# Kernel tuning notes

Measured on AMD Instinct MI355X. Metric: run time of the kernel, lower is better.

## Reference

```python
import jax, jax.numpy as jnp
import numpy as np

DIM = 128
DIM_OUT = 128
TK = 3   # time kernel (causal)
SK = 3   # spatial kernel
EPS = 1e-8


def setup_inputs() -> dict:
    key = jax.random.key(0)
    k1, k2, k3 = jax.random.split(key, 3)
    fmap = jax.random.normal(k1, (4, DIM, 16, 64, 64), dtype=jnp.float32)
    cond = jax.random.normal(k2, (4, DIM), dtype=jnp.float32)
    fan_in = DIM * TK * SK * SK
    gain = 0.75  # kaiming gain for selu
    weights = jax.random.normal(k3, (DIM_OUT, DIM, TK, SK, SK), dtype=jnp.float32) * (gain / np.sqrt(fan_in))
    return {"fmap": fmap, "cond": cond, "weights": weights}


def reference(fmap, cond, weights):
    # per-sample weight modulation: w[b,o,i,kt,kh,kw] = W[o,i,...] * (cond[b,i] + 1)
    w = weights[None] * (cond[:, None, :, None, None, None] + 1.0)
    # demodulation: normalize per (b, o) over (i, kt, kh, kw)
    ssq = jnp.sum(w * w, axis=(2, 3, 4, 5), keepdims=True)
    w = w * jax.lax.rsqrt(jnp.maximum(ssq, EPS))
    # causal time padding (TK-1, 0), symmetric spatial padding SK//2
    sp = SK // 2
    fmap_p = jnp.pad(fmap, ((0, 0), (0, 0), (TK - 1, 0), (sp, sp), (sp, sp)))
    # per-sample conv3d (equivalent to groups=b grouped conv)
    dn = ('NCDHW', 'OIDHW', 'NCDHW')
    def conv_one(x, wi):
        # x: [c, t, h, w], wi: [o, i, kt, kh, kw]
        return jax.lax.conv_general_dilated(
            x[None], wi, window_strides=(1, 1, 1), padding='VALID',
            dimension_numbers=dn)[0]
    return jax.vmap(conv_one)(fmap_p, w)  # [b, o, t, h, w]
```

## Files before the change

kernel.cpp:

```cpp
#include <hip/hip_runtime.h>

typedef float f32x4 __attribute__((ext_vector_type(4)));
typedef short s16x8 __attribute__((ext_vector_type(8)));

#define NB 4
#define CIN 128
#define COUT 128
#define NT 16
#define NH 64
#define NW 64
#define NTAP 27
#define KTOT (CIN * NTAP)

#define FT_H 66
#define FT_W 66
#define WMOD_BYTES (NB * NTAP * COUT * CIN * 2)
#define FT_U16 ((size_t)NB * NT * FT_H * FT_W * CIN)
#define FT_BYTES (FT_U16 * 2)
#define WS_NEED ((size_t)WMOD_BYTES + FT_BYTES)

#define SFT 4
#define SFH 6
#define SFW 66
#define SFPX (SFT * SFH * SFW)
#define SF_SLOTS (SFPX * 4)

#define VMCNT0() asm volatile("s_waitcnt vmcnt(0)" ::: "memory")
#define LGKM0()  asm volatile("s_waitcnt lgkmcnt(0)" ::: "memory")
#define BARRIER() asm volatile("s_barrier" ::: "memory")

__device__ __forceinline__ unsigned short f32_to_bf16(float f) {
    unsigned int u = __builtin_bit_cast(unsigned int, f);
    u += 0x7FFFu + ((u >> 16) & 1u);
    return (unsigned short)(u >> 16);
}

__device__ __forceinline__ void gload16(const void* g, void* l) {
    __builtin_amdgcn_global_load_lds(
        (const __attribute__((address_space(1))) unsigned int*)g,
        (__attribute__((address_space(3))) unsigned int*)l, 16, 0, 0);
}

__global__ __launch_bounds__(256) void modw_kernel(
    const float* __restrict__ cond,
    const float* __restrict__ weights,
    unsigned short* __restrict__ wmod,
    int swz)
{
    int bo = blockIdx.x;
    int b = bo >> 7;
    int o = bo & 127;
    int tid = threadIdx.x;
    __shared__ float red[256];
    __shared__ float s_scale;
    const float* wrow = weights + o * KTOT;
    const float* cb = cond + b * CIN;

    float acc = 0.f;
    for (int idx = tid; idx < KTOT; idx += 256) {
        int i = idx / NTAP;
        float v = wrow[idx] * (cb[i] + 1.0f);
        acc += v * v;
    }
    red[tid] = acc;
    __syncthreads();
    #pragma unroll
    for (int s = 128; s > 0; s >>= 1) {
        if (tid < s) red[tid] += red[tid + s];
        __syncthreads();
    }
    if (tid == 0) s_scale = 1.0f / sqrtf(fmaxf(red[0], 1e-8f));
    __syncthreads();
    float scale = s_scale;
    int sw_o = swz ? ((o >> 1) & 3) : 0;

    for (int idx = tid; idx < KTOT; idx += 256) {
        int i = idx / NTAP;
        int tap = idx - i * NTAP;
        float v = wrow[idx] * (cb[i] + 1.0f) * scale;
        int pos = (i & 0x60) | ((((i >> 3) & 3) ^ sw_o) << 3) | (i & 7);
        wmod[(((b * NTAP + tap) * COUT + o) * CIN) + pos] = f32_to_bf16(v);
    }
}

__global__ void border_kernel(unsigned short* __restrict__ fmapT) {
    int idx = blockIdx.x * blockDim.x + threadIdx.x;
    int total = NB * NT * 260 * 16;
    if (idx >= total) return;
    int slot = idx & 15;
    int pid = idx >> 4;
    int r = pid % 260;
    int bt = pid / 260;
    int hh, ww;
    if (r < 66)       { hh = 0;  ww = r; }
    else if (r < 132) { hh = 65; ww = r - 66; }
    else if (r < 196) { ww = 0;  hh = r - 131; }
    else              { ww = 65; hh = r - 195; }
    size_t p = (((size_t)bt * FT_H + hh) * FT_W + ww) * CIN + slot * 8;
    uint4 z = {0, 0, 0, 0};
    *reinterpret_cast<uint4*>(&fmapT[p]) = z;
}

__global__ __launch_bounds__(256) void transpose_kernel(
    const float* __restrict__ fmap, unsigned short* __restrict__ fmapT)
{
    __shared__ __attribute__((aligned(16))) unsigned short sT[NW * 136];
    int bid = blockIdx.x;
    int h = bid & 63;
    int t = (bid >> 6) & 15;
    int b = bid >> 10;
    int tid = threadIdx.x;

    int c = tid >> 1, wh = (tid & 1) * 32;
    const float* src = fmap + (((size_t)(b * CIN + c) * NT + t) * NH + h) * NW + wh;
    #pragma unroll
    for (int j = 0; j < 8; ++j) {
        float4 v = *reinterpret_cast<const float4*>(src + j * 4);
        int w = wh + j * 4;
        sT[(w + 0) * 136 + c] = f32_to_bf16(v.x);
        sT[(w + 1) * 136 + c] = f32_to_bf16(v.y);
        sT[(w + 2) * 136 + c] = f32_to_bf16(v.z);
        sT[(w + 3) * 136 + c] = f32_to_bf16(v.w);
    }
    __syncthreads();

    int w = tid >> 2, qq = tid & 3;
    int sw = ((w + 1) >> 1) & 3;
    size_t pixbase = (((size_t)(b * NT + t) * FT_H + (h + 1)) * FT_W + (w + 1)) * CIN;
    #pragma unroll
    for (int s = 0; s < 4; ++s) {
        int g = qq * 4 + s;
        uint4 v = *reinterpret_cast<const uint4*>(&sT[w * 136 + g * 8]);
        int slot = (g & 12) | ((g & 3) ^ sw);
        *reinterpret_cast<uint4*>(&fmapT[pixbase + slot * 8]) = v;
    }
}

__global__ __launch_bounds__(512, 2) void conv2_kernel(
    const unsigned short* __restrict__ fmapT,
    const unsigned short* __restrict__ wmod,
    float* __restrict__ out)
{
    __shared__ __attribute__((aligned(16))) unsigned short sF[SFPX * 32];

    int obid = blockIdx.x;
    int bid = (obid & 7) * 64 + (obid >> 3);
    int h0 = (bid & 15) * 4;
    int t0 = ((bid >> 4) & 7) * 2;
    int b  = bid >> 7;

    int tid = threadIdx.x;
    int wv = tid >> 6;
    int l  = tid & 63;
    int lo = l & 15, hi = l >> 4;
    int obase = (wv & 1) * 64;
    int tsub  = (wv >> 1) & 1;
    int hp    = (wv >> 2) * 2;

    f32x4 acc[4][2][4];
    f32x4 zz = {0.f, 0.f, 0.f, 0.f};
    #pragma unroll
    for (int a = 0; a < 4; ++a)
        #pragma unroll
        for (int h2 = 0; h2 < 2; ++h2)
            #pragma unroll
            for (int p = 0; p < 4; ++p)
                acc[a][h2][p] = zz;

    int nz = (t0 == 0) ? (2 * SFH * SFW * 4) : 0;

    auto stage_f = [&](int ic) {
        #pragma unroll 1
        for (int j = 0; j < 13; ++j) {
            int s = j * 512 + tid;
            if (s < SF_SLOTS) {
                int px = s >> 2, q = s & 3;
                int row = px / SFW;
                int wl = px - row * SFW;
                int tl = row / SFH;
                int hl = row - tl * SFH;
                int ts = t0 + tl - 2;
                if (ts < 0) ts = 0;
                const unsigned short* src = fmapT +
                    ((((size_t)(b * NT + ts) * FT_H + (h0 + hl)) * FT_W + wl) << 7)
                    + (ic << 5) + (q << 3);
                gload16(src, &sF[(size_t)s * 8]);
            }
        }
    };
    auto zero_t = [&]() {
        uint4 z = {0, 0, 0, 0};
        for (int s = tid; s < nz; s += 512)
            *reinterpret_cast<uint4*>(&sF[(size_t)s * 8]) = z;
    };

    const unsigned short* wlane = wmod
        + ((size_t)b * NTAP * COUT) * CIN
        + (obase + lo) * CIN + hi * 8;

    int offk[3];
    #pragma unroll
    for (int kw = 0; kw < 3; ++kw)
        offk[kw] = ((kw + lo) << 5) + ((hi ^ (((lo + kw) >> 1) & 3)) << 3);

    #pragma unroll 1
    for (int ic = 0; ic < 4; ++ic) {
        if (ic) {
            LGKM0();
            BARRIER();
        }
        stage_f(ic);
        const unsigned short* wch = wlane + (ic << 5);

        s16x8 afb[2][4];
        #pragma unroll
        for (int a = 0; a < 4; ++a)
            afb[0][a] = *reinterpret_cast<const s16x8*>(wch + a * 16 * CIN);

        VMCNT0();
        if (nz) zero_t();
        LGKM0();
        BARRIER();

        #pragma unroll
        for (int tap = 0; tap < 27; ++tap) {
            int kt = tap / 9;
            int kh = (tap / 3) % 3;
            int kw = tap % 3;

            if (tap < 26) {
                const unsigned short* wnxt = wch + (size_t)(tap + 1) * (COUT * CIN);
                #pragma unroll
                for (int a = 0; a < 4; ++a)
                    afb[(tap + 1) & 1][a] =
                        *reinterpret_cast<const s16x8*>(wnxt + a * 16 * CIN);
            }

            int rb = ((tsub + kt) * SFH + hp + kh) * (SFW * 32) + offk[kw];
            s16x8 bf[2][4];
            #pragma unroll
            for (int h2 = 0; h2 < 2; ++h2)
                #pragma unroll
                for (int p = 0; p < 4; ++p)
                    bf[h2][p] = *reinterpret_cast<const s16x8*>(
                        &sF[rb + h2 * (SFW * 32) + p * 512]);

            #pragma unroll
            for (int h2 = 0; h2 < 2; ++h2)
                #pragma unroll
                for (int a = 0; a < 4; ++a)
                    #pragma unroll
                    for (int p = 0; p < 4; ++p)
                        acc[a][h2][p] = __builtin_amdgcn_mfma_f32_16x16x32_bf16(
                            afb[tap & 1][a], bf[h2][p], acc[a][h2][p], 0, 0, 0);
        }
    }

    int t = t0 + tsub;
    #pragma unroll
    for (int a = 0; a < 4; ++a) {
        #pragma unroll
        for (int h2 = 0; h2 < 2; ++h2) {
            int h = h0 + hp + h2;
            #pragma unroll
            for (int reg = 0; reg < 4; ++reg) {
                int o = obase + a * 16 + hi * 4 + reg;
                float* orow = out + ((((size_t)b * COUT + o) * NT + t) * NH + h) * NW;
                #pragma unroll
                for (int p = 0; p < 4; ++p)
                    orow[p * 16 + lo] = acc[a][h2][p][reg];
            }
        }
    }
}

#define HB 4
#define SF_T 3
#define SF_Hf (HB + 2)
#define SF_Wf (NW + 2)
#define IPAD 40
#define SPATf (SF_T * SF_Hf * SF_Wf)

__global__ __launch_bounds__(512) void conv_kernel(
    const float* __restrict__ fmap,
    const unsigned short* __restrict__ wmod,
    float* __restrict__ out)
{
    __shared__ unsigned short sFf[SPATf * IPAD];
    __shared__ unsigned short sWf[2][COUT * IPAD];

    int bid = blockIdx.x;
    int h0 = (bid & 15) * HB;
    int t0 = (bid >> 4) & 15;
    int b  = bid >> 8;

    int tid = threadIdx.x;
    int wv = tid >> 6;
    int l  = tid & 63;
    int lo = l & 15;
    int hi = l >> 4;
    int obase = (wv & 1) * 64;
    int r = wv >> 1;

    int s_ii = tid >> 4;
    int s_ws = tid & 15;

    f32x4 acc[4][4];
    #pragma unroll
    for (int a = 0; a < 4; ++a)
        #pragma unroll
        for (int p = 0; p < 4; ++p)
            acc[a][p] = f32x4{0.f, 0.f, 0.f, 0.f};

    int tap = 0, icc = 0;
    for (int ks = 0; ks < 108; ++ks) {
        if (tap == 0) {
            if (ks) __syncthreads();
            const float* fbase = fmap + (size_t)((b * CIN + icc * 32 + s_ii) * NT) * (NH * NW);
            for (int e = s_ws; e < SPATf; e += 16) {
                int wl = e % SF_Wf;
                int rr = e / SF_Wf;
                int hl = rr % SF_Hf;
                int tl = rr / SF_Hf;
                int ts = t0 + tl - 2;
                int hs = h0 + hl - 1;
                int wsrc = wl - 1;
                float v = 0.f;
                if (ts >= 0 && (unsigned)hs < NH && (unsigned)wsrc < NW)
                    v = fbase[(ts * NH + hs) * NW + wsrc];
                sFf[e * IPAD + s_ii] = f32_to_bf16(v);
            }
            if (ks == 0) {
                int o = tid >> 2, q = tid & 3;
                const unsigned short* src =
                    wmod + (((b * NTAP + 0) * COUT + o) * CIN) + q * 8;
                *reinterpret_cast<uint4*>(&sWf[0][o * IPAD + q * 8]) =
                    *reinterpret_cast<const uint4*>(src);
            }
        }
        __syncthreads();

        if (ks + 1 < 108) {
            int ksn = ks + 1;
            int icn = ksn / 27;
            int tapn = ksn - icn * 27;
            int o = tid >> 2, q = tid & 3;
            const unsigned short* src =
                wmod + (((b * NTAP + tapn) * COUT + o) * CIN) + icn * 32 + q * 8;
            *reinterpret_cast<uint4*>(&sWf[ksn & 1][o * IPAD + q * 8]) =
                *reinterpret_cast<const uint4*>(src);
        }

        int kt = tap / 9;
        int rem = tap - kt * 9;
        int kh = rem / 3;
        int kw = rem - kh * 3;

        s16x8 af[4], bfr[4];
        #pragma unroll
        for (int a = 0; a < 4; ++a) {
            int o = obase + a * 16 + lo;
            af[a] = *reinterpret_cast<const s16x8*>(&sWf[ks & 1][o * IPAD + hi * 8]);
        }
        #pragma unroll
        for (int p = 0; p < 4; ++p) {
            int sp = (kt * SF_Hf + (r + kh)) * SF_Wf + (p * 16 + lo + kw);
            bfr[p] = *reinterpret_cast<const s16x8*>(&sFf[sp * IPAD + hi * 8]);
        }
        #pragma unroll
        for (int a = 0; a < 4; ++a)
            #pragma unroll
            for (int p = 0; p < 4; ++p)
                acc[a][p] = __builtin_amdgcn_mfma_f32_16x16x32_bf16(
                    af[a], bfr[p], acc[a][p], 0, 0, 0);

        if (++tap == 27) { tap = 0; ++icc; }
    }

    int h = h0 + r;
    #pragma unroll
    for (int a = 0; a < 4; ++a) {
        #pragma unroll
        for (int reg = 0; reg < 4; ++reg) {
            int o = obase + a * 16 + hi * 4 + reg;
            float* orow = out + ((((size_t)b * COUT + o) * NT + t0) * NH + h) * NW;
            #pragma unroll
            for (int p = 0; p < 4; ++p)
                orow[p * 16 + lo] = acc[a][p][reg];
        }
    }
}

extern "C" void kernel_launch(void* const* d_in, const int* in_sizes, int n_in,
                              void* d_out, int out_size, void* d_ws, size_t ws_size,
                              hipStream_t stream) {
    (void)in_sizes; (void)n_in; (void)out_size;
    const float* fmap    = (const float*)d_in[0];
    const float* cond    = (const float*)d_in[1];
    const float* weights = (const float*)d_in[2];
    float* outp = (float*)d_out;
    unsigned short* wmod = (unsigned short*)d_ws;

    if (ws_size >= WS_NEED) {
        unsigned short* fmapT = (unsigned short*)((char*)d_ws + WMOD_BYTES);
        modw_kernel<<<dim3(NB * COUT), dim3(256), 0, stream>>>(cond, weights, wmod, 0);
        border_kernel<<<dim3((NB * NT * 260 * 16 + 255) / 256), dim3(256), 0, stream>>>(fmapT);
        transpose_kernel<<<dim3(NB * NT * NH), dim3(256), 0, stream>>>(fmap, fmapT);
        conv2_kernel<<<dim3(NB * (NT / 2) * (NH / 4)), dim3(512), 0, stream>>>(fmapT, wmod, outp);
    } else {
        modw_kernel<<<dim3(NB * COUT), dim3(256), 0, stream>>>(cond, weights, wmod, 0);
        conv_kernel<<<dim3(NB * NT * (NH / HB)), dim3(512), 0, stream>>>(fmap, wmod, outp);
    }
}
```

Baseline: 302.4 us.

## Stagger per-wave tap order and software-pipeline LDS feature loads across MFMAs

Each wave now starts its 27-tap loop at a different rotation (roff), so waves read different weight slices and LDS rows at the same moment. The intent is to spread global/L2 weight traffic and LDS bank accesses instead of having every wave hit the same tap together. The feature fragments are also double-buffered per spatial column p, with the next column loaded while the current MFMAs run, which lowers peak VGPR use for B operands. The costs are that tap indices are no longer compile-time constants, so kt/kh/kw and the offsets are computed at runtime, and LDS latency may be exposed more often.

Measured after the change: 318.0 us. 1.05x slower.

```diff
diff --git a/kernel.cpp b/kernel.cpp
--- a/kernel.cpp
+++ b/kernel.cpp
@@ -156,6 +156,7 @@
     int obase = (wv & 1) * 64;
     int tsub  = (wv >> 1) & 1;
     int hp    = (wv >> 2) * 2;
+    int roff  = (wv & 3) * 6;
 
     f32x4 acc[4][2][4];
     f32x4 zz = {0.f, 0.f, 0.f, 0.f};
@@ -198,11 +199,6 @@
         + ((size_t)b * NTAP * COUT) * CIN
         + (obase + lo) * CIN + hi * 8;
 
-    int offk[3];
-    #pragma unroll
-    for (int kw = 0; kw < 3; ++kw)
-        offk[kw] = ((kw + lo) << 5) + ((hi ^ (((lo + kw) >> 1) & 3)) << 3);
-
     #pragma unroll 1
     for (int ic = 0; ic < 4; ++ic) {
         if (ic) {
@@ -213,9 +209,12 @@
         const unsigned short* wch = wlane + (ic << 5);
 
         s16x8 afb[2][4];
-        #pragma unroll
-        for (int a = 0; a < 4; ++a)
-            afb[0][a] = *reinterpret_cast<const s16x8*>(wch + a * 16 * CIN);
+        {
+            const unsigned short* w0 = wch + (size_t)roff * (COUT * CIN);
+            #pragma unroll
+            for (int a = 0; a < 4; ++a)
+                afb[0][a] = *reinterpret_cast<const s16x8*>(w0 + a * 16 * CIN);
+        }
 
         VMCNT0();
         if (nz) zero_t();
@@ -223,36 +222,43 @@
         BARRIER();
 
         #pragma unroll
-        for (int tap = 0; tap < 27; ++tap) {
+        for (int idx = 0; idx < 27; ++idx) {
+            int tap = idx + roff; if (tap >= NTAP) tap -= NTAP;
             int kt = tap / 9;
             int kh = (tap / 3) % 3;
             int kw = tap % 3;
 
-            if (tap < 26) {
-                const unsigned short* wnxt = wch + (size_t)(tap + 1) * (COUT * CIN);
+            if (idx < 26) {
+                int tapn = idx + 1 + roff; if (tapn >= NTAP) tapn -= NTAP;
+                const unsigned short* wnxt = wch + (size_t)tapn * (COUT * CIN);
                 #pragma unroll
                 for (int a = 0; a < 4; ++a)
-                    afb[(tap + 1) & 1][a] =
+                    afb[(idx + 1) & 1][a] =
                         *reinterpret_cast<const s16x8*>(wnxt + a * 16 * CIN);
             }
 
-            int rb = ((tsub + kt) * SFH + hp + kh) * (SFW * 32) + offk[kw];
-            s16x8 bf[2][4];
-            #pragma unroll
-            for (int h2 = 0; h2 < 2; ++h2)
+            int off = ((kw + lo) << 5) + ((hi ^ (((lo + kw) >> 1) & 3)) << 3);
+            int rb = ((tsub + kt) * SFH + hp + kh) * (SFW * 32) + off;
+
+            s16x8 bfp[2][2];
+            bfp[0][0] = *reinterpret_cast<const s16x8*>(&sF[rb]);
+            bfp[0][1] = *reinterpret_cast<const s16x8*>(&sF[rb + SFW * 32]);
+
+            #pragma unroll
+            for (int p = 0; p < 4; ++p) {
+                if (p < 3) {
+                    bfp[(p + 1) & 1][0] = *reinterpret_cast<const s16x8*>(
+                        &sF[rb + (p + 1) * 512]);
+                    bfp[(p + 1) & 1][1] = *reinterpret_cast<const s16x8*>(
+                        &sF[rb + SFW * 32 + (p + 1) * 512]);
+                }
                 #pragma unroll
-                for (int p = 0; p < 4; ++p)
-                    bf[h2][p] = *reinterpret_cast<const s16x8*>(
-                        &sF[rb + h2 * (SFW * 32) + p * 512]);
-
-            #pragma unroll
-            for (int h2 = 0; h2 < 2; ++h2)
-                #pragma unroll
-                for (int a = 0; a < 4; ++a)
+                for (int h2 = 0; h2 < 2; ++h2)
                     #pragma unroll
-                    for (int p = 0; p < 4; ++p)
+                    for (int a = 0; a < 4; ++a)
                         acc[a][h2][p] = __builtin_amdgcn_mfma_f32_16x16x32_bf16(
-                            afb[tap & 1][a], bf[h2][p], acc[a][h2][p], 0, 0, 0);
+                            afb[idx & 1][a], bfp[p & 1][h2], acc[a][h2][p], 0, 0, 0);
+            }
         }
     }
 
```

## Shrink conv tile to one time step and two rows with 256-thread blocks

Applied to the files above, without the earlier changes.

Replaces the 512-thread conv2 kernel, which covered a 2x4 (t,h) output tile, with a 256-thread conv3 kernel covering one time step and two output rows. Each wave now holds a quarter of the accumulators, and the launch bound asks for three blocks per CU. The aim is better occupancy, a smaller LDS footprint and more blocks for load balance. The cost is less reuse of the staged input: the time and row halos are now reloaded for every smaller tile, so global-to-LDS traffic per output rises.

New measurement: 482.6 us. +59.6%, slower.

```diff
diff --git a/kernel.cpp b/kernel.cpp
--- a/kernel.cpp
+++ b/kernel.cpp
@@ -19,15 +19,14 @@
 #define FT_BYTES (FT_U16 * 2)
 #define WS_NEED ((size_t)WMOD_BYTES + FT_BYTES)
 
-#define SFT 4
-#define SFH 6
-#define SFW 66
-#define SFPX (SFT * SFH * SFW)
-#define SF_SLOTS (SFPX * 4)
+#define S3_PX_USED (3 * 4 * FT_W)
+#define S3_PX 832
+#define S3_SLOTS (S3_PX * 4)
+#define S3_LDS_U16 (S3_PX * 32)
 
 #define VMCNT0() asm volatile("s_waitcnt vmcnt(0)" ::: "memory")
 #define LGKM0()  asm volatile("s_waitcnt lgkmcnt(0)" ::: "memory")
-#define BARRIER() asm volatile("s_barrier" ::: "memory")
+#define BARRIER() __builtin_amdgcn_s_barrier()
 
 __device__ __forceinline__ unsigned short f32_to_bf16(float f) {
     unsigned int u = __builtin_bit_cast(unsigned int, f);
@@ -136,61 +135,58 @@
     }
 }
 
-__global__ __launch_bounds__(512, 2) void conv2_kernel(
+__global__ __launch_bounds__(256, 3) void conv3_kernel(
     const unsigned short* __restrict__ fmapT,
     const unsigned short* __restrict__ wmod,
     float* __restrict__ out)
 {
-    __shared__ __attribute__((aligned(16))) unsigned short sF[SFPX * 32];
+    __shared__ __attribute__((aligned(16))) unsigned short sF[S3_LDS_U16];
 
     int obid = blockIdx.x;
-    int bid = (obid & 7) * 64 + (obid >> 3);
-    int h0 = (bid & 15) * 4;
-    int t0 = ((bid >> 4) & 7) * 2;
-    int b  = bid >> 7;
+    int bid = (obid & 7) * 256 + (obid >> 3);
+    int h0 = bid & 31;
+    int t0 = (bid >> 5) & 15;
+    int b  = bid >> 9;
 
     int tid = threadIdx.x;
     int wv = tid >> 6;
     int l  = tid & 63;
     int lo = l & 15, hi = l >> 4;
     int obase = (wv & 1) * 64;
-    int tsub  = (wv >> 1) & 1;
-    int hp    = (wv >> 2) * 2;
-
-    f32x4 acc[4][2][4];
+    int hsub  = wv >> 1;
+
+    f32x4 acc[4][4];
     f32x4 zz = {0.f, 0.f, 0.f, 0.f};
     #pragma unroll
     for (int a = 0; a < 4; ++a)
         #pragma unroll
-        for (int h2 = 0; h2 < 2; ++h2)
-            #pragma unroll
-            for (int p = 0; p < 4; ++p)
-                acc[a][h2][p] = zz;
-
-    int nz = (t0 == 0) ? (2 * SFH * SFW * 4) : 0;
+        for (int p = 0; p < 4; ++p)
+            acc[a][p] = zz;
+
+    int nzp = (t0 < 2) ? (2 - t0) : 0;
+    int nz = nzp * 4 * FT_W * 4;
 
     auto stage_f = [&](int ic) {
         #pragma unroll 1
         for (int j = 0; j < 13; ++j) {
-            int s = j * 512 + tid;
-            if (s < SF_SLOTS) {
-                int px = s >> 2, q = s & 3;
-                int row = px / SFW;
-                int wl = px - row * SFW;
-                int tl = row / SFH;
-                int hl = row - tl * SFH;
-                int ts = t0 + tl - 2;
-                if (ts < 0) ts = 0;
-                const unsigned short* src = fmapT +
-                    ((((size_t)(b * NT + ts) * FT_H + (h0 + hl)) * FT_W + wl) << 7)
-                    + (ic << 5) + (q << 3);
-                gload16(src, &sF[(size_t)s * 8]);
-            }
+            int s = j * 256 + tid;
+            int px = s >> 2, q = s & 3;
+            if (px > S3_PX_USED - 1) px = S3_PX_USED - 1;
+            int row = px / FT_W;
+            int wl = px - row * FT_W;
+            int tl = row >> 2;
+            int hl = row & 3;
+            int ts = t0 + tl - 2;
+            if (ts < 0) ts = 0;
+            const unsigned short* src = fmapT +
+                ((((size_t)(b * NT + ts) * FT_H + (2 * h0 + hl)) * FT_W + wl) << 7)
+                + (ic << 5) + (q << 3);
+            gload16(src, &sF[(size_t)s * 8]);
         }
     };
     auto zero_t = [&]() {
         uint4 z = {0, 0, 0, 0};
-        for (int s = tid; s < nz; s += 512)
+        for (int s = tid; s < nz; s += 256)
             *reinterpret_cast<uint4*>(&sF[(size_t)s * 8]) = z;
     };
 
@@ -212,10 +208,10 @@
         stage_f(ic);
         const unsigned short* wch = wlane + (ic << 5);
 
-        s16x8 afb[2][4];
+        s16x8 aN[2][4];
         #pragma unroll
         for (int a = 0; a < 4; ++a)
-            afb[0][a] = *reinterpret_cast<const s16x8*>(wch + a * 16 * CIN);
+            aN[0][a] = *reinterpret_cast<const s16x8*>(wch + a * 16 * CIN);
 
         VMCNT0();
         if (nz) zero_t();
@@ -224,52 +220,43 @@
 
         #pragma unroll
         for (int tap = 0; tap < 27; ++tap) {
-            int kt = tap / 9;
-            int kh = (tap / 3) % 3;
-            int kw = tap % 3;
+            const int cur = tap & 1;
+            const int kt = tap / 9;
+            const int kh = (tap / 3) % 3;
+            const int kw = tap % 3;
 
             if (tap < 26) {
                 const unsigned short* wnxt = wch + (size_t)(tap + 1) * (COUT * CIN);
                 #pragma unroll
                 for (int a = 0; a < 4; ++a)
-                    afb[(tap + 1) & 1][a] =
-                        *reinterpret_cast<const s16x8*>(wnxt + a * 16 * CIN);
+                    aN[cur ^ 1][a] = *reinterpret_cast<const s16x8*>(wnxt + a * 16 * CIN);
             }
 
-            int rb = ((tsub + kt) * SFH + hp + kh) * (SFW * 32) + offk[kw];
-            s16x8 bf[2][4];
+            int rb = (kt * 4 + hsub + kh) * (FT_W * 32) + offk[kw];
+            s16x8 bf[4];
             #pragma unroll
-            for (int h2 = 0; h2 < 2; ++h2)
+            for (int p = 0; p < 4; ++p)
+                bf[p] = *reinterpret_cast<const s16x8*>(&sF[rb + p * 512]);
+
+            #pragma unroll
+            for (int a = 0; a < 4; ++a)
                 #pragma unroll
                 for (int p = 0; p < 4; ++p)
-                    bf[h2][p] = *reinterpret_cast<const s16x8*>(
-                        &sF[rb + h2 * (SFW * 32) + p * 512]);
-
+                    acc[a][p] = __builtin_amdgcn_mfma_f32_16x16x32_bf16(
+                        aN[cur][a], bf[p], acc[a][p], 0, 0, 0);
+        }
+    }
+
+    int h = 2 * h0 + hsub;
+    #pragma unroll
+    for (int a = 0; a < 4; ++a) {
+        #pragma unroll
+        for (int reg = 0; reg < 4; ++reg) {
+            int o = obase + a * 16 + hi * 4 + reg;
+            float* orow = out + ((((size_t)b * COUT + o) * NT + t0) * NH + h) * NW;
             #pragma unroll
-            for (int h2 = 0; h2 < 2; ++h2)
-                #pragma unroll
-                for (int a = 0; a < 4; ++a)
-                    #pragma unroll
-                    for (int p = 0; p < 4; ++p)
-                        acc[a][h2][p] = __builtin_amdgcn_mfma_f32_16x16x32_bf16(
-                            afb[tap & 1][a], bf[h2][p], acc[a][h2][p], 0, 0, 0);
-        }
-    }
-
-    int t = t0 + tsub;
-    #pragma unroll
-    for (int a = 0; a < 4; ++a) {
-        #pragma unroll
-        for (int h2 = 0; h2 < 2; ++h2) {
-            int h = h0 + hp + h2;
-            #pragma unroll
-            for (int reg = 0; reg < 4; ++reg) {
-                int o = obase + a * 16 + hi * 4 + reg;
-                float* orow = out + ((((size_t)b * COUT + o) * NT + t) * NH + h) * NW;
-                #pragma unroll
-                for (int p = 0; p < 4; ++p)
-                    orow[p * 16 + lo] = acc[a][h2][p][reg];
-            }
+            for (int p = 0; p < 4; ++p)
+                orow[p * 16 + lo] = acc[a][p][reg];
         }
     }
 }
@@ -406,7 +393,7 @@
         modw_kernel<<<dim3(NB * COUT), dim3(256), 0, stream>>>(cond, weights, wmod, 0);
         border_kernel<<<dim3((NB * NT * 260 * 16 + 255) / 256), dim3(256), 0, stream>>>(fmapT);
         transpose_kernel<<<dim3(NB * NT * NH), dim3(256), 0, stream>>>(fmap, fmapT);
-        conv2_kernel<<<dim3(NB * (NT / 2) * (NH / 4)), dim3(512), 0, stream>>>(fmapT, wmod, outp);
+        conv3_kernel<<<dim3(NB * NT * 32), dim3(256), 0, stream>>>(fmapT, wmod, outp);
     } else {
         modw_kernel<<<dim3(NB * COUT), dim3(256), 0, stream>>>(cond, weights, wmod, 0);
         conv_kernel<<<dim3(NB * NT * (NH / HB)), dim3(512), 0, stream>>>(fmap, wmod, outp);
```
